# Performance work log

Hardware: AMD Instinct MI355X
Metric: run time of the kernel (lower is better)

The kernel has to match this reference:

```python
import jax, jax.numpy as jnp
import numpy as np

DIVERSITY = 1.0
DISPARITY_STEP = 2


def setup_inputs() -> dict:
    key = jax.random.key(0)
    k1, k2, k3 = jax.random.split(key, 3)
    B, D, H, W = 8, 64, 256, 512
    similarities = jax.random.normal(k1, (B, D, H, W), dtype=jnp.float32)
    max_disp = (D - 1) * DISPARITY_STEP  # 126
    gt = jax.random.uniform(k2, (B, H, W), dtype=jnp.float32) * max_disp
    unknown = jax.random.uniform(k3, (B, H, W)) < 0.05
    gt = jnp.where(unknown, jnp.inf, gt)
    return {"similarities": similarities, "ground_truth_disparities": gt}


def reference(similarities, ground_truth_disparities):
    # similarities: [B, D, H, W]; ground_truth_disparities: [B, H, W]
    D = similarities.shape[1]
    known = jnp.isfinite(ground_truth_disparities)           # [B, H, W]
    gt_safe = jnp.where(known, ground_truth_disparities, 0.0)
    log_P_pred = jax.nn.log_softmax(similarities, axis=1)    # [B, D, H, W]
    disparities = (jnp.arange(D, dtype=similarities.dtype)
                   * DISPARITY_STEP)[None, :, None, None]    # [1, D, 1, 1]
    # Unnormalized Laplace target centered at sub-pixel ground truth
    P_target = jnp.exp(-jnp.abs(gt_safe[:, None] - disparities) / DIVERSITY) \
               / (2.0 * DIVERSITY)                            # [B, D, H, W]
    sum_P_target = jnp.sum(P_target, axis=1)                  # [B, H, W]
    sum_Pt_logP = jnp.sum(P_target * log_P_pred, axis=1)      # [B, H, W]
    entropy = -sum_Pt_logP / sum_P_target                     # [B, H, W]
    # Mean over pixels with known ground truth (masked mean, jit-friendly)
    num_known = jnp.sum(known)
    return jnp.sum(jnp.where(known, entropy, 0.0)) / num_known
```

## Files before the change

kernel.cpp:

```cpp
#include <hip/hip_runtime.h>
#include <math.h>

constexpr int Bn = 8, Dn = 64, Hn = 256, Wn = 512;
constexpr int HW   = Hn * Wn;
constexpr int NPIX = Bn * HW;
constexpr int TPB  = 256;
constexpr int PPT  = 4;
constexpr int NBLK = NPIX / (TPB * PPT);
constexpr int UF   = 8;
constexpr int NG   = Dn / UF;

typedef float fx4 __attribute__((ext_vector_type(4)));

__global__ __launch_bounds__(TPB) void sce_main(const float* __restrict__ sim,
                                                const float* __restrict__ gt,
                                                float* __restrict__ accf,
                                                unsigned* __restrict__ ticket,
                                                float* __restrict__ out) {
    const int tid = blockIdx.x * TPB + threadIdx.x;
    const int p0  = tid * PPT;
    const int b   = p0 / HW;
    const int rem = p0 - b * HW;
    const fx4* simv = reinterpret_cast<const fx4*>(sim + (size_t)b * Dn * HW + rem);
    const int ds = HW / 4;

    const fx4 g4 = __builtin_nontemporal_load(reinterpret_cast<const fx4*>(gt + p0));
    float gg[4] = {g4.x, g4.y, g4.z, g4.w};

    float s[4]  = {0.f, 0.f, 0.f, 0.f};
    float S1[4] = {0.f, 0.f, 0.f, 0.f};
    float S2[4] = {0.f, 0.f, 0.f, 0.f};

    fx4 cur[UF], nxt[UF];
#pragma unroll
    for (int i = 0; i < UF; ++i)
        cur[i] = __builtin_nontemporal_load(&simv[(size_t)i * ds]);

#pragma unroll
    for (int g = 0; g < NG; ++g) {
        if (g + 1 < NG) {
#pragma unroll
            for (int i = 0; i < UF; ++i)
                nxt[i] = __builtin_nontemporal_load(&simv[(size_t)((g + 1) * UF + i) * ds]);
        }
#pragma unroll
        for (int i = 0; i < UF; ++i) {
            const float dd = 2.0f * (float)(g * UF + i);
            float v[4] = {cur[i].x, cur[i].y, cur[i].z, cur[i].w};
#pragma unroll
            for (int j = 0; j < 4; ++j) {
                s[j] += __expf(v[j]);
                float t = __expf(-fabsf(gg[j] - dd));
                S1[j] += t;
                S2[j] = fmaf(t, v[j], S2[j]);
            }
        }
#pragma unroll
        for (int i = 0; i < UF; ++i) cur[i] = nxt[i];
    }

    float lsum = 0.0f, lcnt = 0.0f;
#pragma unroll
    for (int j = 0; j < 4; ++j) {
        if (isfinite(gg[j])) {
            lsum += __logf(s[j]) - S2[j] / S1[j];
            lcnt += 1.0f;
        }
    }

#pragma unroll
    for (int off = 32; off > 0; off >>= 1) {
        lsum += __shfl_down(lsum, off, 64);
        lcnt += __shfl_down(lcnt, off, 64);
    }

    __shared__ float ssum[TPB / 64], scnt[TPB / 64];
    const int lane = threadIdx.x & 63;
    const int wave = threadIdx.x >> 6;
    if (lane == 0) { ssum[wave] = lsum; scnt[wave] = lcnt; }
    __syncthreads();
    if (threadIdx.x == 0) {
        float bs = 0.f, bc = 0.f;
#pragma unroll
        for (int w = 0; w < TPB / 64; ++w) { bs += ssum[w]; bc += scnt[w]; }
        atomicAdd(&accf[0], bs);
        atomicAdd(&accf[1], bc);
        __threadfence();
        unsigned old = atomicAdd(ticket, 1u);
        if (old == NBLK - 1) {
            __threadfence();
            float ts = atomicAdd(&accf[0], 0.0f);
            float tc = atomicAdd(&accf[1], 0.0f);
            out[0] = ts / tc;
        }
    }
}

extern "C" void kernel_launch(void* const* d_in, const int* in_sizes, int n_in,
                              void* d_out, int out_size, void* d_ws, size_t ws_size,
                              hipStream_t stream) {
    const float* sim = (const float*)d_in[0];
    const float* gt  = (const float*)d_in[1];
    float* accf = (float*)d_ws;
    unsigned* ticket = (unsigned*)d_ws + 2;
    hipMemsetAsync(d_ws, 0, 16, stream);
    sce_main<<<NBLK, TPB, 0, stream>>>(sim, gt, accf, ticket, (float*)d_out);
}
```

Before: 374.9 us.

## Split disparity axis across waves and replace per-element Laplace exp with scaled products

Each block now covers 256 pixels, and each of its four waves handles a quarter of the disparity range. All 16 vector loads per thread are issued up front, and partial sums are combined through shared memory before one wave finishes the pixel entropy. The Laplace weight exp(-|g-d|) is now the minimum of two running products (a per-thread precomputed exp times a compile-time constant), which drops one transcendental per element. This raises the block count and memory-level parallelism and cuts ALU work. The cost is shared-memory traffic, a barrier, and possible overflow or underflow in the product form, which is masked by fminf and by the small target values involved.

```diff
diff --git a/kernel.cpp b/kernel.cpp
--- a/kernel.cpp
+++ b/kernel.cpp
@@ -5,10 +5,9 @@
 constexpr int HW   = Hn * Wn;
 constexpr int NPIX = Bn * HW;
 constexpr int TPB  = 256;
-constexpr int PPT  = 4;
-constexpr int NBLK = NPIX / (TPB * PPT);
-constexpr int UF   = 8;
-constexpr int NG   = Dn / UF;
+constexpr int PXB  = 256;
+constexpr int NBLK = NPIX / PXB;
+constexpr int DPW  = Dn / 4;
 
 typedef float fx4 __attribute__((ext_vector_type(4)));
 
@@ -17,81 +16,90 @@
                                                 float* __restrict__ accf,
                                                 unsigned* __restrict__ ticket,
                                                 float* __restrict__ out) {
-    const int tid = blockIdx.x * TPB + threadIdx.x;
-    const int p0  = tid * PPT;
-    const int b   = p0 / HW;
-    const int rem = p0 - b * HW;
-    const fx4* simv = reinterpret_cast<const fx4*>(sim + (size_t)b * Dn * HW + rem);
-    const int ds = HW / 4;
+    const int lane = threadIdx.x & 63;
+    const int wave = threadIdx.x >> 6;
+    const int p0   = blockIdx.x * PXB + lane * 4;
+    const int b    = p0 / HW;
+    const int rem  = p0 - b * HW;
+    const float* base = sim + (size_t)b * Dn * HW + rem;
+    const int d0 = wave * DPW;
 
-    const fx4 g4 = __builtin_nontemporal_load(reinterpret_cast<const fx4*>(gt + p0));
+    const fx4 g4 = *reinterpret_cast<const fx4*>(gt + p0);
     float gg[4] = {g4.x, g4.y, g4.z, g4.w};
+
+    float Pa[4], Pb[4];
+#pragma unroll
+    for (int j = 0; j < 4; ++j) {
+        Pa[j] = __expf(gg[j] - 2.0f * (float)d0);
+        Pb[j] = __expf(2.0f * (float)d0 - gg[j]);
+    }
+
+    fx4 v0[8], v1[8];
+#pragma unroll
+    for (int i = 0; i < 8; ++i)
+        v0[i] = __builtin_nontemporal_load(
+            reinterpret_cast<const fx4*>(base + (size_t)(d0 + i) * HW));
+#pragma unroll
+    for (int i = 0; i < 8; ++i)
+        v1[i] = __builtin_nontemporal_load(
+            reinterpret_cast<const fx4*>(base + (size_t)(d0 + 8 + i) * HW));
 
     float s[4]  = {0.f, 0.f, 0.f, 0.f};
     float S1[4] = {0.f, 0.f, 0.f, 0.f};
     float S2[4] = {0.f, 0.f, 0.f, 0.f};
 
-    fx4 cur[UF], nxt[UF];
 #pragma unroll
-    for (int i = 0; i < UF; ++i)
-        cur[i] = __builtin_nontemporal_load(&simv[(size_t)i * ds]);
+    for (int i = 0; i < DPW; ++i) {
+        const fx4 vv = (i < 8) ? v0[i & 7] : v1[i & 7];
+        const float ra = __builtin_expf(-2.0f * (float)i);
+        const float rb = __builtin_expf( 2.0f * (float)i);
+        float v[4] = {vv.x, vv.y, vv.z, vv.w};
+#pragma unroll
+        for (int j = 0; j < 4; ++j) {
+            s[j] += __expf(v[j]);
+            float t = fminf(Pa[j] * ra, Pb[j] * rb);
+            S1[j] += t;
+            S2[j] = fmaf(t, v[j], S2[j]);
+        }
+    }
 
+    __shared__ float red[4][12][64];
 #pragma unroll
-    for (int g = 0; g < NG; ++g) {
-        if (g + 1 < NG) {
+    for (int j = 0; j < 4; ++j) {
+        red[wave][j][lane]     = s[j];
+        red[wave][4 + j][lane] = S1[j];
+        red[wave][8 + j][lane] = S2[j];
+    }
+    __syncthreads();
+
+    if (wave == 0) {
+        float lsum = 0.f, lcnt = 0.f;
 #pragma unroll
-            for (int i = 0; i < UF; ++i)
-                nxt[i] = __builtin_nontemporal_load(&simv[(size_t)((g + 1) * UF + i) * ds]);
-        }
-#pragma unroll
-        for (int i = 0; i < UF; ++i) {
-            const float dd = 2.0f * (float)(g * UF + i);
-            float v[4] = {cur[i].x, cur[i].y, cur[i].z, cur[i].w};
-#pragma unroll
-            for (int j = 0; j < 4; ++j) {
-                s[j] += __expf(v[j]);
-                float t = __expf(-fabsf(gg[j] - dd));
-                S1[j] += t;
-                S2[j] = fmaf(t, v[j], S2[j]);
+        for (int j = 0; j < 4; ++j) {
+            float st = red[0][j][lane] + red[1][j][lane] + red[2][j][lane] + red[3][j][lane];
+            float s1 = red[0][4+j][lane] + red[1][4+j][lane] + red[2][4+j][lane] + red[3][4+j][lane];
+            float s2 = red[0][8+j][lane] + red[1][8+j][lane] + red[2][8+j][lane] + red[3][8+j][lane];
+            if (isfinite(gg[j])) {
+                lsum += __logf(st) - s2 / s1;
+                lcnt += 1.0f;
             }
         }
 #pragma unroll
-        for (int i = 0; i < UF; ++i) cur[i] = nxt[i];
-    }
-
-    float lsum = 0.0f, lcnt = 0.0f;
-#pragma unroll
-    for (int j = 0; j < 4; ++j) {
-        if (isfinite(gg[j])) {
-            lsum += __logf(s[j]) - S2[j] / S1[j];
-            lcnt += 1.0f;
+        for (int off = 32; off > 0; off >>= 1) {
+            lsum += __shfl_down(lsum, off, 64);
+            lcnt += __shfl_down(lcnt, off, 64);
         }
-    }
-
-#pragma unroll
-    for (int off = 32; off > 0; off >>= 1) {
-        lsum += __shfl_down(lsum, off, 64);
-        lcnt += __shfl_down(lcnt, off, 64);
-    }
-
-    __shared__ float ssum[TPB / 64], scnt[TPB / 64];
-    const int lane = threadIdx.x & 63;
-    const int wave = threadIdx.x >> 6;
-    if (lane == 0) { ssum[wave] = lsum; scnt[wave] = lcnt; }
-    __syncthreads();
-    if (threadIdx.x == 0) {
-        float bs = 0.f, bc = 0.f;
-#pragma unroll
-        for (int w = 0; w < TPB / 64; ++w) { bs += ssum[w]; bc += scnt[w]; }
-        atomicAdd(&accf[0], bs);
-        atomicAdd(&accf[1], bc);
-        __threadfence();
-        unsigned old = atomicAdd(ticket, 1u);
-        if (old == NBLK - 1) {
+        if (lane == 0) {
+            atomicAdd(&accf[0], lsum);
+            atomicAdd(&accf[1], lcnt);
             __threadfence();
-            float ts = atomicAdd(&accf[0], 0.0f);
-            float tc = atomicAdd(&accf[1], 0.0f);
-            out[0] = ts / tc;
+            unsigned old = atomicAdd(ticket, 1u);
+            if (old == NBLK - 1) {
+                __threadfence();
+                float ts = atomicAdd(&accf[0], 0.0f);
+                float tc = atomicAdd(&accf[1], 0.0f);
+                out[0] = ts / tc;
+            }
         }
     }
 }
```

Result: slower. 535.2 us (+42.8%).

## Factor Laplace target exp into per-pixel and per-disparity terms, deepen load batches

Applied to the files above, without the earlier changes.

Replaces the per-element exp(-|gt - d|) with fmin of two products. Each product combines a per-pixel factor exp(±(gt-64)) with a per-disparity constant exp(∓2(d-32)). This removes one transcendental per element, leaving only the softmax exp. The prefetch batch grows from 8 to 16 float4 loads, the kernel gets a launch_bounds occupancy hint of 2, and nontemporal loads become plain loads. The factored form relies on float overflow and underflow behaving sanely. Larger register use for the batch could lower occupancy.

```diff
diff --git a/kernel.cpp b/kernel.cpp
--- a/kernel.cpp
+++ b/kernel.cpp
@@ -2,61 +2,70 @@
 #include <math.h>
 
 constexpr int Bn = 8, Dn = 64, Hn = 256, Wn = 512;
-constexpr int HW   = Hn * Wn;
-constexpr int NPIX = Bn * HW;
-constexpr int TPB  = 256;
-constexpr int PPT  = 4;
-constexpr int NBLK = NPIX / (TPB * PPT);
-constexpr int UF   = 8;
-constexpr int NG   = Dn / UF;
+constexpr int HW    = Hn * Wn;
+constexpr int NPIX  = Bn * HW;
+constexpr int TPB   = 256;
+constexpr int PPT   = 4;
+constexpr int NBLK  = NPIX / (TPB * PPT);
+constexpr int BATCH = 16;
+constexpr int NB    = Dn / BATCH;
 
 typedef float fx4 __attribute__((ext_vector_type(4)));
 
-__global__ __launch_bounds__(TPB) void sce_main(const float* __restrict__ sim,
-                                                const float* __restrict__ gt,
-                                                float* __restrict__ accf,
-                                                unsigned* __restrict__ ticket,
-                                                float* __restrict__ out) {
+__global__ __launch_bounds__(TPB, 2) void sce_main(const float* __restrict__ sim,
+                                                   const float* __restrict__ gt,
+                                                   float* __restrict__ accf,
+                                                   unsigned* __restrict__ ticket,
+                                                   float* __restrict__ out) {
     const int tid = blockIdx.x * TPB + threadIdx.x;
     const int p0  = tid * PPT;
     const int b   = p0 / HW;
     const int rem = p0 - b * HW;
-    const fx4* simv = reinterpret_cast<const fx4*>(sim + (size_t)b * Dn * HW + rem);
-    const int ds = HW / 4;
+    const float* base = sim + (size_t)b * Dn * HW + rem;
 
-    const fx4 g4 = __builtin_nontemporal_load(reinterpret_cast<const fx4*>(gt + p0));
+    const fx4 g4 = *reinterpret_cast<const fx4*>(gt + p0);
     float gg[4] = {g4.x, g4.y, g4.z, g4.w};
+
+    float Pa[4], Pb[4];
+#pragma unroll
+    for (int j = 0; j < 4; ++j) {
+        Pa[j] = __expf(gg[j] - 64.0f);
+        Pb[j] = __expf(64.0f - gg[j]);
+    }
 
     float s[4]  = {0.f, 0.f, 0.f, 0.f};
     float S1[4] = {0.f, 0.f, 0.f, 0.f};
     float S2[4] = {0.f, 0.f, 0.f, 0.f};
 
-    fx4 cur[UF], nxt[UF];
+    fx4 cur[BATCH], nxt[BATCH];
 #pragma unroll
-    for (int i = 0; i < UF; ++i)
-        cur[i] = __builtin_nontemporal_load(&simv[(size_t)i * ds]);
+    for (int i = 0; i < BATCH; ++i)
+        cur[i] = *reinterpret_cast<const fx4*>(base + (size_t)i * HW);
 
 #pragma unroll
-    for (int g = 0; g < NG; ++g) {
-        if (g + 1 < NG) {
+    for (int g = 0; g < NB; ++g) {
+        if (g + 1 < NB) {
 #pragma unroll
-            for (int i = 0; i < UF; ++i)
-                nxt[i] = __builtin_nontemporal_load(&simv[(size_t)((g + 1) * UF + i) * ds]);
+            for (int i = 0; i < BATCH; ++i)
+                nxt[i] = *reinterpret_cast<const fx4*>(
+                    base + (size_t)((g + 1) * BATCH + i) * HW);
         }
 #pragma unroll
-        for (int i = 0; i < UF; ++i) {
-            const float dd = 2.0f * (float)(g * UF + i);
+        for (int i = 0; i < BATCH; ++i) {
+            const int d = g * BATCH + i;
+            const float ra = __builtin_expf(-2.0f * (float)(d - 32));
+            const float rb = __builtin_expf( 2.0f * (float)(d - 32));
             float v[4] = {cur[i].x, cur[i].y, cur[i].z, cur[i].w};
 #pragma unroll
             for (int j = 0; j < 4; ++j) {
                 s[j] += __expf(v[j]);
-                float t = __expf(-fabsf(gg[j] - dd));
+                float t = fminf(Pa[j] * ra, Pb[j] * rb);
                 S1[j] += t;
                 S2[j] = fmaf(t, v[j], S2[j]);
             }
         }
 #pragma unroll
-        for (int i = 0; i < UF; ++i) cur[i] = nxt[i];
+        for (int i = 0; i < BATCH; ++i) cur[i] = nxt[i];
     }
 
     float lsum = 0.0f, lcnt = 0.0f;
```

After: 501.1 us. 33.7% more time.
